# Kernel optimization log

Measured on AMD Instinct MI355X. Metric: run time of the kernel, lower is better.

Reference implementation:

```python
import jax, jax.numpy as jnp
import numpy as np

N_NODES = 50000
N_EDGES = 1600000
NODE_DIM = 64
EDGE_DIM = 32
UNITS = 64


def _glorot(key, shape):
    fan_in, fan_out = shape[0], shape[1]
    lim = jnp.sqrt(6.0 / (fan_in + fan_out))
    return jax.random.uniform(key, shape, jnp.float32, -lim, lim)


def setup_inputs() -> dict:
    key = jax.random.key(0)
    ks = jax.random.split(key, 16)
    msg_in = 2 * NODE_DIM + EDGE_DIM  # concat(sender, receiver, edge)
    upd_in = NODE_DIM + UNITS         # concat(node, aggregated)
    return {
        "node_features": jax.random.normal(ks[0], (N_NODES, NODE_DIM), jnp.float32),
        "edge_features": jax.random.normal(ks[1], (N_EDGES, EDGE_DIM), jnp.float32),
        "senders": jax.random.randint(ks[2], (N_EDGES,), 0, N_NODES, jnp.int32),
        "receivers": jnp.sort(jax.random.randint(ks[3], (N_EDGES,), 0, N_NODES, jnp.int32)),
        # message_net
        "W1": _glorot(ks[4], (msg_in, UNITS)), "b1": jnp.zeros((UNITS,), jnp.float32),
        "W2": _glorot(ks[5], (UNITS, UNITS)), "b2": jnp.zeros((UNITS,), jnp.float32),
        # attention_net
        "Wa1": _glorot(ks[6], (msg_in, UNITS)), "ba1": jnp.zeros((UNITS,), jnp.float32),
        "Wa2": _glorot(ks[7], (UNITS, 1)), "ba2": jnp.zeros((1,), jnp.float32),
        # update_net
        "Wu1": _glorot(ks[8], (upd_in, UNITS)), "bu1": jnp.zeros((UNITS,), jnp.float32),
        "Wu2": _glorot(ks[9], (UNITS, UNITS)), "bu2": jnp.zeros((UNITS,), jnp.float32),
    }


def reference(node_features, edge_features, senders, receivers,
              W1, b1, W2, b2, Wa1, ba1, Wa2, ba2, Wu1, bu1, Wu2, bu2):
    act = jax.nn.swish
    # gather + concat: [E, 2*node_dim + edge_dim]
    msg_in = jnp.concatenate(
        [node_features[senders], node_features[receivers], edge_features], axis=-1)
    # message MLP
    messages = act(msg_in @ W1 + b1) @ W2 + b2  # [E, units]
    # attention: softmax over ALL edges (axis=0), as in the original
    att_logits = act(msg_in @ Wa1 + ba1) @ Wa2 + ba2  # [E, 1]
    att = jax.nn.softmax(att_logits, axis=0)
    messages = messages * att
    # scatter-sum to receivers
    aggregated = jax.ops.segment_sum(messages, receivers, num_segments=node_features.shape[0])
    upd_in = jnp.concatenate([node_features, aggregated], axis=-1)
    return act(upd_in @ Wu1 + bu1) @ Wu2 + bu2  # [N, units]
```

## Files before the change

kernel.cpp:

```cpp
#include <hip/hip_runtime.h>
#include <cstdint>
#include <cstddef>

#define N_NODES_C 50000
#define N_EDGES_C 1600000

typedef __attribute__((ext_vector_type(8)))  short bf16x8;
typedef __attribute__((ext_vector_type(16))) float f32x16;
typedef unsigned short ushort_t;

static const size_t AGG_OFF   = 512;
static const size_t NB_OFF    = 512 + (size_t)N_NODES_C * 64 * 4;
static const size_t WIMG_OFF  = NB_OFF + (size_t)N_NODES_C * 64 * 2;
static const size_t WUIMG_OFF = WIMG_OFF + 49152;

__device__ __forceinline__ float swish_(float v) { return v / (1.0f + __expf(-v)); }

__device__ __forceinline__ unsigned short f2bf(float f) {
    unsigned int u = __float_as_uint(f);
    return (unsigned short)((u + 0x7FFFu + ((u >> 16) & 1u)) >> 16);
}
__device__ __forceinline__ unsigned int pack2(float a, float b) {
    return (unsigned int)f2bf(a) | ((unsigned int)f2bf(b) << 16);
}
__device__ __forceinline__ bf16x8 pack8(float4 a, float4 b) {
    union { uint4 u; bf16x8 v; } un;
    un.u.x = pack2(a.x, a.y); un.u.y = pack2(a.z, a.w);
    un.u.z = pack2(b.x, b.y); un.u.w = pack2(b.z, b.w);
    return un.v;
}

typedef __attribute__((address_space(3))) unsigned int lds_u32_t;
typedef const __attribute__((address_space(1))) unsigned int glb_u32_t;
__device__ __forceinline__ void glds16(const void* g, void* l) {
    __builtin_amdgcn_global_load_lds((glb_u32_t*)g, (lds_u32_t*)l, 16, 0, 0);
}

__global__ __launch_bounds__(256) void k_prep_node(const float* __restrict__ node,
                                                   ushort_t* __restrict__ node_bf)
{
    int i = blockIdx.x * 256 + threadIdx.x;
    if (i >= N_NODES_C * 64 / 8) return;
    const float4* s = (const float4*)node + (size_t)i * 2;
    float4 a = s[0], b = s[1];
    uint4 p = { pack2(a.x,a.y), pack2(a.z,a.w), pack2(b.x,b.y), pack2(b.z,b.w) };
    ((uint4*)node_bf)[i] = p;
}

__global__ __launch_bounds__(256) void k_prep_w(
    const float* __restrict__ W1, const float* __restrict__ Wa1,
    const float* __restrict__ W2, const float* __restrict__ Wu1,
    const float* __restrict__ Wu2,
    ushort_t* __restrict__ wm, ushort_t* __restrict__ wa, ushort_t* __restrict__ w2s,
    ushort_t* __restrict__ wu1t, ushort_t* __restrict__ wu2t)
{
    int b = blockIdx.x, t = threadIdx.x;
    if (b < 20) {
        int p = b * 256 + t; int n = p / 80, j = p - n * 80;
        ((unsigned int*)wm)[n * 80 + j] = pack2(W1[(size_t)(2*j) * 64 + n], W1[(size_t)(2*j+1) * 64 + n]);
    } else if (b < 40) {
        int p = (b - 20) * 256 + t; int n = p / 80, j = p - n * 80;
        ((unsigned int*)wa)[n * 80 + j] = pack2(Wa1[(size_t)(2*j) * 64 + n], Wa1[(size_t)(2*j+1) * 64 + n]);
    } else if (b < 48) {
        int p = (b - 40) * 256 + t; int n = p >> 5, q = p & 31, c = q >> 2, j = q & 3;
        ((unsigned int*)w2s)[n * 32 + ((c ^ (n & 7)) << 2) + j] =
            pack2(W2[(size_t)(c*4 + j) * 64 + n], W2[(size_t)(c*4 + j + 32) * 64 + n]);
    } else if (b < 65) {
        int p = (b - 48) * 256 + t; int n = p / 68, j = p - n * 68; int k2 = 2 * j;
        unsigned int v = (k2 < 128) ? pack2(Wu1[(size_t)k2 * 64 + n], Wu1[(size_t)(k2+1) * 64 + n]) : 0u;
        ((unsigned int*)wu1t)[n * 68 + j] = v;
    } else {
        int p = (b - 65) * 256 + t; int n = p / 36, j = p - n * 36; int k2 = 2 * j;
        unsigned int v = (k2 < 64) ? pack2(Wu2[(size_t)k2 * 64 + n], Wu2[(size_t)(k2+1) * 64 + n]) : 0u;
        ((unsigned int*)wu2t)[n * 36 + j] = v;
    }
}

__global__ __launch_bounds__(256, 2) void k_edge(
    const ushort_t* __restrict__ node_bf, const float* __restrict__ edgef,
    const int* __restrict__ senders, const int* __restrict__ receivers,
    const ushort_t* __restrict__ wimg,
    const float* __restrict__ b1, const float* __restrict__ ba1,
    const float* __restrict__ Wa2, const float* __restrict__ ba2,
    const float* __restrict__ b2,
    float* __restrict__ expsum, float* __restrict__ agg)
{
    __shared__ ushort_t SMEM[40960];
    ushort_t* As  = SMEM;
    ushort_t* Ar  = SMEM + 8192;
    ushort_t* Wm  = SMEM + 16384;
    ushort_t* Wa  = SMEM + 26624;
    ushort_t* W2s = SMEM + 36864;

    const int tid = threadIdx.x;
    const int e0 = blockIdx.x * 128;
    const int lane = tid & 63, w = tid >> 6;
    const int lr = lane & 31, hi = lane >> 5, kh = hi * 8;

    for (int c = tid; c < 2560; c += 256)
        glds16((const char*)wimg + c * 16, (char*)Wm + c * 16);
    for (int c = tid; c < 512; c += 256)
        glds16((const char*)wimg + 40960 + c * 16, (char*)W2s + c * 16);
    #pragma unroll
    for (int i = 0; i < 4; ++i) {
        int cg = tid + i * 256;
        int row = cg >> 3, c = cg & 7;
        glds16(node_bf + (size_t)senders[e0 + row] * 64 + ((c ^ (row & 7)) << 3),
               (char*)As + cg * 16);
    }
    #pragma unroll
    for (int i = 0; i < 4; ++i) {
        int cg = tid + i * 256;
        int row = cg >> 3, c = cg & 7;
        glds16(node_bf + (size_t)receivers[e0 + row] * 64 + ((c ^ (row & 7)) << 3),
               (char*)Ar + cg * 16);
    }
    bf16x8 ae0, ae1;
    {
        const float4* ep = (const float4*)(edgef + (size_t)(e0 + w * 32 + lr) * 32);
        ae0 = pack8(ep[2 * hi], ep[2 * hi + 1]);
        ae1 = pack8(ep[4 + 2 * hi], ep[4 + 2 * hi + 1]);
    }
    __syncthreads();

    f32x16 ca0, ca1, cm0, cm1;
    #pragma unroll
    for (int j = 0; j < 16; ++j) { ca0[j]=0.f; ca1[j]=0.f; cm0[j]=0.f; cm1[j]=0.f; }
    const ushort_t* asr = As + (w * 32 + lr) * 64;
    const ushort_t* arr = Ar + (w * 32 + lr) * 64;
    const ushort_t* wm0 = Wm + lr * 160 + kh;
    const ushort_t* wm1 = Wm + (32 + lr) * 160 + kh;
    const ushort_t* wa0 = Wa + lr * 160 + kh;
    const ushort_t* wa1 = Wa + (32 + lr) * 160 + kh;
    #pragma unroll
    for (int kk = 0; kk < 4; ++kk) {
        bf16x8 a = *(const bf16x8*)(asr + (((2*kk + hi) ^ (lr & 7)) << 3));
        cm0 = __builtin_amdgcn_mfma_f32_32x32x16_bf16(a, *(const bf16x8*)(wm0 + kk*16), cm0, 0,0,0);
        cm1 = __builtin_amdgcn_mfma_f32_32x32x16_bf16(a, *(const bf16x8*)(wm1 + kk*16), cm1, 0,0,0);
        ca0 = __builtin_amdgcn_mfma_f32_32x32x16_bf16(a, *(const bf16x8*)(wa0 + kk*16), ca0, 0,0,0);
        ca1 = __builtin_amdgcn_mfma_f32_32x32x16_bf16(a, *(const bf16x8*)(wa1 + kk*16), ca1, 0,0,0);
    }
    #pragma unroll
    for (int kk = 4; kk < 8; ++kk) {
        bf16x8 a = *(const bf16x8*)(arr + (((2*(kk-4) + hi) ^ (lr & 7)) << 3));
        cm0 = __builtin_amdgcn_mfma_f32_32x32x16_bf16(a, *(const bf16x8*)(wm0 + kk*16), cm0, 0,0,0);
        cm1 = __builtin_amdgcn_mfma_f32_32x32x16_bf16(a, *(const bf16x8*)(wm1 + kk*16), cm1, 0,0,0);
        ca0 = __builtin_amdgcn_mfma_f32_32x32x16_bf16(a, *(const bf16x8*)(wa0 + kk*16), ca0, 0,0,0);
        ca1 = __builtin_amdgcn_mfma_f32_32x32x16_bf16(a, *(const bf16x8*)(wa1 + kk*16), ca1, 0,0,0);
    }
    {
        bf16x8 a = ae0;
        cm0 = __builtin_amdgcn_mfma_f32_32x32x16_bf16(a, *(const bf16x8*)(wm0 + 128), cm0, 0,0,0);
        cm1 = __builtin_amdgcn_mfma_f32_32x32x16_bf16(a, *(const bf16x8*)(wm1 + 128), cm1, 0,0,0);
        ca0 = __builtin_amdgcn_mfma_f32_32x32x16_bf16(a, *(const bf16x8*)(wa0 + 128), ca0, 0,0,0);
        ca1 = __builtin_amdgcn_mfma_f32_32x32x16_bf16(a, *(const bf16x8*)(wa1 + 128), ca1, 0,0,0);
        a = ae1;
        cm0 = __builtin_amdgcn_mfma_f32_32x32x16_bf16(a, *(const bf16x8*)(wm0 + 144), cm0, 0,0,0);
        cm1 = __builtin_amdgcn_mfma_f32_32x32x16_bf16(a, *(const bf16x8*)(wm1 + 144), cm1, 0,0,0);
        ca0 = __builtin_amdgcn_mfma_f32_32x32x16_bf16(a, *(const bf16x8*)(wa0 + 144), ca0, 0,0,0);
        ca1 = __builtin_amdgcn_mfma_f32_32x32x16_bf16(a, *(const bf16x8*)(wa1 + 144), ca1, 0,0,0);
    }
    __syncthreads();

    ushort_t* H = Wa;
    const float bb0 = ba1[lr], bb1 = ba1[32 + lr];
    const float wv0 = Wa2[lr], wv1 = Wa2[32 + lr];
    #pragma unroll
    for (int t = 0; t < 16; ++t) {
        int r = (t & 3) + 8 * (t >> 2) + 4 * hi;
        *(unsigned int*)(H + (w * 32 + r) * 72 + 2 * lr) =
            pack2(swish_(ca0[t] + bb0) * wv0, swish_(ca1[t] + bb1) * wv1);
    }
    f32x16 da;
    #pragma unroll
    for (int j = 0; j < 16; ++j) da[j] = 0.f;
    bf16x8 ones;
    #pragma unroll
    for (int i = 0; i < 8; ++i) ones[i] = (short)0x3F80;
    const ushort_t* hp = H + (w * 32 + lr) * 72 + kh;
    #pragma unroll
    for (int kk = 0; kk < 4; ++kk)
        da = __builtin_amdgcn_mfma_f32_32x32x16_bf16(*(const bf16x8*)(hp + kk*16), ones, da, 0,0,0);

    const float ba2v = ba2[0];
    float p[16];
    float ps = 0.f;
    #pragma unroll
    for (int t = 0; t < 16; ++t) { p[t] = __expf(da[t] + ba2v); ps += p[t]; }
    ps += __shfl_xor(ps, 1);  ps += __shfl_xor(ps, 2);  ps += __shfl_xor(ps, 4);
    ps += __shfl_xor(ps, 8);  ps += __shfl_xor(ps, 16); ps += __shfl_xor(ps, 32);
    if (lane == 0) atomicAdd(&expsum[w * 16], ps * 0.03125f);

    const float b10 = b1[lr], b11 = b1[32 + lr];
    #pragma unroll
    for (int t = 0; t < 16; ++t) {
        int r = (t & 3) + 8 * (t >> 2) + 4 * hi;
        *(unsigned int*)(H + (w * 32 + r) * 72 + 2 * lr) =
            pack2(swish_(cm0[t] + b10), swish_(cm1[t] + b11));
    }
    f32x16 d0, d1;
    #pragma unroll
    for (int j = 0; j < 16; ++j) { d0[j] = 0.f; d1[j] = 0.f; }
    const ushort_t* q0 = W2s + lr * 64;
    const ushort_t* q1 = W2s + (32 + lr) * 64;
    #pragma unroll
    for (int kk = 0; kk < 4; ++kk) {
        bf16x8 a = *(const bf16x8*)(hp + kk * 16);
        int sw = ((2*kk + hi) ^ (lr & 7)) << 3;
        d0 = __builtin_amdgcn_mfma_f32_32x32x16_bf16(a, *(const bf16x8*)(q0 + sw), d0, 0,0,0);
        d1 = __builtin_amdgcn_mfma_f32_32x32x16_bf16(a, *(const bf16x8*)(q1 + sw), d1, 0,0,0);
    }

    float* Msc = (float*)SMEM;
    const float b20 = b2[lr], b21 = b2[32 + lr];
    #pragma unroll
    for (int t = 0; t < 16; ++t) {
        int r = (t & 3) + 8 * (t >> 2) + 4 * hi;
        float2 mv = { (d0[t] + b20) * p[t], (d1[t] + b21) * p[t] };
        *(float2*)(Msc + (w * 32 + r) * 64 + 2 * lr) = mv;
    }
    const int cj = (lane < 32) ? 2 * lane : 2 * (lane - 32) + 1;
    const int ews = e0 + w * 32;
    float acc = 0.f;
    int cur = receivers[ews];
    #pragma unroll 4
    for (int i = 0; i < 32; ++i) {
        int rr = receivers[ews + i];
        if (rr != cur) {
            atomicAdd(&agg[(size_t)cur * 64 + lane], acc);
            acc = 0.f; cur = rr;
        }
        acc += Msc[(w * 32 + i) * 64 + cj];
    }
    atomicAdd(&agg[(size_t)cur * 64 + lane], acc);
}

__global__ __launch_bounds__(256) void k_upd(
    const ushort_t* __restrict__ node_bf, const float* __restrict__ agg,
    const ushort_t* __restrict__ wuimg,
    const float* __restrict__ bu1, const float* __restrict__ bu2,
    const float* __restrict__ expsum, float* __restrict__ out)
{
    __shared__ ushort_t Un[128 * 64];
    __shared__ ushort_t Ua[128 * 64];
    __shared__ ushort_t Wu[13312];
    __shared__ ushort_t H2[128 * 72];

    const int tid = threadIdx.x;
    const int n0 = blockIdx.x * 128;

    for (int c = tid; c < 1664; c += 256)
        glds16((const char*)wuimg + c * 16, (char*)Wu + c * 16);
    #pragma unroll
    for (int i = 0; i < 4; ++i) {
        int cg = tid + i * 256;
        int row = cg >> 3, c = cg & 7;
        int n = n0 + row; if (n >= N_NODES_C) n = N_NODES_C - 1;
        glds16(node_bf + (size_t)n * 64 + ((c ^ (row & 7)) << 3), (char*)Un + cg * 16);
    }
    float z = 0.f;
    #pragma unroll
    for (int q = 0; q < 8; ++q) z += expsum[q * 16];
    const float invZ = 1.0f / z;
    {
        int row = tid >> 1, hf = tid & 1;
        int n = n0 + row; if (n >= N_NODES_C) n = N_NODES_C - 1;
        const float4* ap = (const float4*)(agg + (size_t)n * 64 + hf * 32);
        int r7 = row & 7;
        #pragma unroll
        for (int q = 0; q < 4; ++q) {
            float4 x = ap[2 * q], y = ap[2 * q + 1];
            uint4 pk = { pack2(x.x * invZ, x.y * invZ), pack2(x.z * invZ, x.w * invZ),
                         pack2(y.x * invZ, y.y * invZ), pack2(y.z * invZ, y.w * invZ) };
            int chunk = hf * 4 + q;
            *(uint4*)(Ua + row * 64 + ((chunk ^ r7) << 3)) = pk;
        }
    }
    __syncthreads();

    const int lane = tid & 63, w = tid >> 6;
    const int lr = lane & 31, hi = lane >> 5, kh = hi * 8;
    const int row_a = w * 32 + lr, r7 = lr & 7;

    f32x16 c0, c1;
    #pragma unroll
    for (int j = 0; j < 16; ++j) { c0[j] = 0.f; c1[j] = 0.f; }
    const ushort_t* un = Un + row_a * 64;
    const ushort_t* ua = Ua + row_a * 64;
    const ushort_t* w10 = Wu + lr * 136 + kh;
    const ushort_t* w11 = Wu + (32 + lr) * 136 + kh;
    #pragma unroll
    for (int kk = 0; kk < 4; ++kk) {
        bf16x8 a = *(const bf16x8*)(un + (((2*kk + hi) ^ r7) << 3));
        c0 = __builtin_amdgcn_mfma_f32_32x32x16_bf16(a, *(const bf16x8*)(w10 + kk*16), c0, 0,0,0);
        c1 = __builtin_amdgcn_mfma_f32_32x32x16_bf16(a, *(const bf16x8*)(w11 + kk*16), c1, 0,0,0);
    }
    #pragma unroll
    for (int kk = 4; kk < 8; ++kk) {
        bf16x8 a = *(const bf16x8*)(ua + (((2*(kk-4) + hi) ^ r7) << 3));
        c0 = __builtin_amdgcn_mfma_f32_32x32x16_bf16(a, *(const bf16x8*)(w10 + kk*16), c0, 0,0,0);
        c1 = __builtin_amdgcn_mfma_f32_32x32x16_bf16(a, *(const bf16x8*)(w11 + kk*16), c1, 0,0,0);
    }
    const float bb0 = bu1[lr], bb1 = bu1[32 + lr];
    #pragma unroll
    for (int t = 0; t < 16; ++t) {
        int r = (t & 3) + 8 * (t >> 2) + 4 * hi;
        int g = (w * 32 + r) * 72;
        H2[g + lr]      = f2bf(swish_(c0[t] + bb0));
        H2[g + 32 + lr] = f2bf(swish_(c1[t] + bb1));
    }
    f32x16 d0, d1;
    #pragma unroll
    for (int j = 0; j < 16; ++j) { d0[j] = 0.f; d1[j] = 0.f; }
    const ushort_t* hp = H2 + row_a * 72 + kh;
    const ushort_t* w20 = Wu + 8704 + lr * 72 + kh;
    const ushort_t* w21 = Wu + 8704 + (32 + lr) * 72 + kh;
    #pragma unroll
    for (int kk = 0; kk < 4; ++kk) {
        bf16x8 a = *(const bf16x8*)(hp + kk * 16);
        d0 = __builtin_amdgcn_mfma_f32_32x32x16_bf16(a, *(const bf16x8*)(w20 + kk*16), d0, 0,0,0);
        d1 = __builtin_amdgcn_mfma_f32_32x32x16_bf16(a, *(const bf16x8*)(w21 + kk*16), d1, 0,0,0);
    }
    const float ob0 = bu2[lr], ob1 = bu2[32 + lr];
    #pragma unroll
    for (int t = 0; t < 16; ++t) {
        int r = (t & 3) + 8 * (t >> 2) + 4 * hi;
        int g = n0 + w * 32 + r;
        if (g < N_NODES_C) {
            out[(size_t)g * 64 + lr]      = d0[t] + ob0;
            out[(size_t)g * 64 + 32 + lr] = d1[t] + ob1;
        }
    }
}

extern "C" void kernel_launch(void* const* d_in, const int* in_sizes, int n_in,
                              void* d_out, int out_size, void* d_ws, size_t ws_size,
                              hipStream_t stream)
{
    const float* node      = (const float*)d_in[0];
    const float* edgef     = (const float*)d_in[1];
    const int*   senders   = (const int*)d_in[2];
    const int*   receivers = (const int*)d_in[3];
    const float* W1  = (const float*)d_in[4];
    const float* b1  = (const float*)d_in[5];
    const float* W2  = (const float*)d_in[6];
    const float* b2  = (const float*)d_in[7];
    const float* Wa1 = (const float*)d_in[8];
    const float* ba1 = (const float*)d_in[9];
    const float* Wa2 = (const float*)d_in[10];
    const float* ba2 = (const float*)d_in[11];
    const float* Wu1 = (const float*)d_in[12];
    const float* bu1 = (const float*)d_in[13];
    const float* Wu2 = (const float*)d_in[14];
    const float* bu2 = (const float*)d_in[15];
    float* out = (float*)d_out;

    char* ws = (char*)d_ws;
    float*    expsum  = (float*)ws;
    float*    agg     = (float*)(ws + AGG_OFF);
    ushort_t* node_bf = (ushort_t*)(ws + NB_OFF);
    ushort_t* wimg    = (ushort_t*)(ws + WIMG_OFF);
    ushort_t* wuimg   = (ushort_t*)(ws + WUIMG_OFF);

    ushort_t* wm   = wimg;
    ushort_t* wa   = wimg + 10240;
    ushort_t* w2s  = wimg + 20480;
    ushort_t* wu1t = wuimg;
    ushort_t* wu2t = wuimg + 8704;

    hipMemsetAsync(ws, 0, AGG_OFF + (size_t)N_NODES_C * 64 * 4, stream);

    k_prep_node<<<(N_NODES_C * 64 / 8 + 255) / 256, 256, 0, stream>>>(node, node_bf);
    k_prep_w<<<74, 256, 0, stream>>>(W1, Wa1, W2, Wu1, Wu2, wm, wa, w2s, wu1t, wu2t);
    k_edge<<<N_EDGES_C / 128, 256, 0, stream>>>(node_bf, edgef, senders, receivers,
                                                wimg, b1, ba1, Wa2, ba2, b2, expsum, agg);
    k_upd<<<(N_NODES_C + 127) / 128, 256, 0, stream>>>(node_bf, agg, wuimg,
                                                       bu1, bu2, expsum, out);
}
```

Before: 631.0 us.

## Make edge kernel persistent with register-prefetched gathers and fused zeroing

The edge kernel becomes persistent: 512 blocks, where each wave walks a contiguous range of 32-edge tiles. Weights are loaded into LDS once per block instead of once per 128-edge block. The next tile's sender, receiver and edge features are gathered directly into registers and issued while the current tile's MFMAs run, and the exp-sum is kept per wave with one atomic at the end. The memset is folded into the node-prep kernel, and the message scratch is now bf16 in LDS rather than fp32. The risks are higher register pressure, reduced precision in the aggregated messages, and possibly lower occupancy for hiding gather latency.

```diff
diff --git a/kernel.cpp b/kernel.cpp
--- a/kernel.cpp
+++ b/kernel.cpp
@@ -4,6 +4,9 @@
 
 #define N_NODES_C 50000
 #define N_EDGES_C 1600000
+#define N_WTILES  50000
+#define N_BLOCKS  512
+#define N_GWAVES  (N_BLOCKS * 4)
 
 typedef __attribute__((ext_vector_type(8)))  short bf16x8;
 typedef __attribute__((ext_vector_type(16))) float f32x16;
@@ -12,7 +15,7 @@
 static const size_t AGG_OFF   = 512;
 static const size_t NB_OFF    = 512 + (size_t)N_NODES_C * 64 * 4;
 static const size_t WIMG_OFF  = NB_OFF + (size_t)N_NODES_C * 64 * 2;
-static const size_t WUIMG_OFF = WIMG_OFF + 49152;
+static const size_t WUIMG_OFF = WIMG_OFF + 51200;
 
 __device__ __forceinline__ float swish_(float v) { return v / (1.0f + __expf(-v)); }
 
@@ -29,6 +32,9 @@
     un.u.z = pack2(b.x, b.y); un.u.w = pack2(b.z, b.w);
     return un.v;
 }
+__device__ __forceinline__ bf16x8 as_bf8(uint4 u) {
+    union { uint4 u; bf16x8 v; } un; un.u = u; return un.v;
+}
 
 typedef __attribute__((address_space(3))) unsigned int lds_u32_t;
 typedef const __attribute__((address_space(1))) unsigned int glb_u32_t;
@@ -37,14 +43,20 @@
 }
 
 __global__ __launch_bounds__(256) void k_prep_node(const float* __restrict__ node,
-                                                   ushort_t* __restrict__ node_bf)
+                                                   ushort_t* __restrict__ node_bf,
+                                                   float* __restrict__ ws_base)
 {
     int i = blockIdx.x * 256 + threadIdx.x;
+    if (blockIdx.x == 0 && threadIdx.x < 128) ws_base[threadIdx.x] = 0.0f;
     if (i >= N_NODES_C * 64 / 8) return;
     const float4* s = (const float4*)node + (size_t)i * 2;
     float4 a = s[0], b = s[1];
     uint4 p = { pack2(a.x,a.y), pack2(a.z,a.w), pack2(b.x,b.y), pack2(b.z,b.w) };
     ((uint4*)node_bf)[i] = p;
+    float4 z = {0.f, 0.f, 0.f, 0.f};
+    float* agg = ws_base + 128;
+    ((float4*)agg)[i * 2]     = z;
+    ((float4*)agg)[i * 2 + 1] = z;
 }
 
 __global__ __launch_bounds__(256) void k_prep_w(
@@ -55,25 +67,49 @@
     ushort_t* __restrict__ wu1t, ushort_t* __restrict__ wu2t)
 {
     int b = blockIdx.x, t = threadIdx.x;
-    if (b < 20) {
-        int p = b * 256 + t; int n = p / 80, j = p - n * 80;
-        ((unsigned int*)wm)[n * 80 + j] = pack2(W1[(size_t)(2*j) * 64 + n], W1[(size_t)(2*j+1) * 64 + n]);
-    } else if (b < 40) {
-        int p = (b - 20) * 256 + t; int n = p / 80, j = p - n * 80;
-        ((unsigned int*)wa)[n * 80 + j] = pack2(Wa1[(size_t)(2*j) * 64 + n], Wa1[(size_t)(2*j+1) * 64 + n]);
-    } else if (b < 48) {
-        int p = (b - 40) * 256 + t; int n = p >> 5, q = p & 31, c = q >> 2, j = q & 3;
-        ((unsigned int*)w2s)[n * 32 + ((c ^ (n & 7)) << 2) + j] =
-            pack2(W2[(size_t)(c*4 + j) * 64 + n], W2[(size_t)(c*4 + j + 32) * 64 + n]);
-    } else if (b < 65) {
-        int p = (b - 48) * 256 + t; int n = p / 68, j = p - n * 68; int k2 = 2 * j;
-        unsigned int v = (k2 < 128) ? pack2(Wu1[(size_t)k2 * 64 + n], Wu1[(size_t)(k2+1) * 64 + n]) : 0u;
-        ((unsigned int*)wu1t)[n * 68 + j] = v;
+    if (b < 21) {
+        int p = b * 256 + t; if (p >= 5376) return;
+        int n = p / 84, j = p - n * 84;
+        unsigned int v = (j < 80) ? pack2(W1[(size_t)(2*j)*64 + n], W1[(size_t)(2*j+1)*64 + n]) : 0u;
+        ((unsigned int*)wm)[p] = v;
+    } else if (b < 42) {
+        int p = (b - 21) * 256 + t; if (p >= 5376) return;
+        int n = p / 84, j = p - n * 84;
+        unsigned int v = (j < 80) ? pack2(Wa1[(size_t)(2*j)*64 + n], Wa1[(size_t)(2*j+1)*64 + n]) : 0u;
+        ((unsigned int*)wa)[p] = v;
+    } else if (b < 50) {
+        int p = (b - 42) * 256 + t;
+        int n = p >> 5, q = p & 31, c = q >> 2, jj = q & 3;
+        ((unsigned int*)w2s)[n * 32 + ((c ^ (n & 7)) << 2) + jj] =
+            pack2(W2[(size_t)(c*4 + jj) * 64 + n], W2[(size_t)(c*4 + jj + 32) * 64 + n]);
+    } else if (b < 67) {
+        int p = (b - 50) * 256 + t; if (p >= 4352) return;
+        int n = p / 68, j = p - n * 68;
+        unsigned int v = (2*j < 128) ? pack2(Wu1[(size_t)(2*j)*64 + n], Wu1[(size_t)(2*j+1)*64 + n]) : 0u;
+        ((unsigned int*)wu1t)[p] = v;
     } else {
-        int p = (b - 65) * 256 + t; int n = p / 36, j = p - n * 36; int k2 = 2 * j;
-        unsigned int v = (k2 < 64) ? pack2(Wu2[(size_t)k2 * 64 + n], Wu2[(size_t)(k2+1) * 64 + n]) : 0u;
-        ((unsigned int*)wu2t)[n * 36 + j] = v;
-    }
+        int p = (b - 67) * 256 + t; if (p >= 2304) return;
+        int n = p / 36, j = p - n * 36;
+        unsigned int v = (2*j < 64) ? pack2(Wu2[(size_t)(2*j)*64 + n], Wu2[(size_t)(2*j+1)*64 + n]) : 0u;
+        ((unsigned int*)wu2t)[p] = v;
+    }
+}
+
+struct EBuf { uint4 sn[4]; uint4 rn[4]; float4 ef[4]; };
+
+__device__ __forceinline__ void issue_data(EBuf& b, const ushort_t* node_bf,
+                                           const float* edgef, int s, int r,
+                                           long e, int hi)
+{
+    const uint4* sp = (const uint4*)(node_bf + (size_t)s * 64);
+    const uint4* rp = (const uint4*)(node_bf + (size_t)r * 64);
+    #pragma unroll
+    for (int kk = 0; kk < 4; ++kk) b.sn[kk] = sp[2 * kk + hi];
+    #pragma unroll
+    for (int kk = 0; kk < 4; ++kk) b.rn[kk] = rp[2 * kk + hi];
+    const float4* ep = (const float4*)(edgef + (size_t)e * 32);
+    b.ef[0] = ep[2 * hi];     b.ef[1] = ep[2 * hi + 1];
+    b.ef[2] = ep[4 + 2 * hi]; b.ef[3] = ep[5 + 2 * hi];
 }
 
 __global__ __launch_bounds__(256, 2) void k_edge(
@@ -85,154 +121,157 @@
     const float* __restrict__ b2,
     float* __restrict__ expsum, float* __restrict__ agg)
 {
-    __shared__ ushort_t SMEM[40960];
-    ushort_t* As  = SMEM;
-    ushort_t* Ar  = SMEM + 8192;
-    ushort_t* Wm  = SMEM + 16384;
-    ushort_t* Wa  = SMEM + 26624;
-    ushort_t* W2s = SMEM + 36864;
+    __shared__ ushort_t SMEM[34816];
+    ushort_t* Wm  = SMEM;
+    ushort_t* Wa  = SMEM + 10752;
+    ushort_t* W2s = SMEM + 21504;
+    ushort_t* H   = SMEM + 25600;
 
     const int tid = threadIdx.x;
-    const int e0 = blockIdx.x * 128;
     const int lane = tid & 63, w = tid >> 6;
     const int lr = lane & 31, hi = lane >> 5, kh = hi * 8;
 
-    for (int c = tid; c < 2560; c += 256)
-        glds16((const char*)wimg + c * 16, (char*)Wm + c * 16);
-    for (int c = tid; c < 512; c += 256)
-        glds16((const char*)wimg + 40960 + c * 16, (char*)W2s + c * 16);
-    #pragma unroll
-    for (int i = 0; i < 4; ++i) {
-        int cg = tid + i * 256;
-        int row = cg >> 3, c = cg & 7;
-        glds16(node_bf + (size_t)senders[e0 + row] * 64 + ((c ^ (row & 7)) << 3),
-               (char*)As + cg * 16);
-    }
-    #pragma unroll
-    for (int i = 0; i < 4; ++i) {
-        int cg = tid + i * 256;
-        int row = cg >> 3, c = cg & 7;
-        glds16(node_bf + (size_t)receivers[e0 + row] * 64 + ((c ^ (row & 7)) << 3),
-               (char*)Ar + cg * 16);
-    }
-    bf16x8 ae0, ae1;
-    {
-        const float4* ep = (const float4*)(edgef + (size_t)(e0 + w * 32 + lr) * 32);
-        ae0 = pack8(ep[2 * hi], ep[2 * hi + 1]);
-        ae1 = pack8(ep[4 + 2 * hi], ep[4 + 2 * hi + 1]);
-    }
+    for (int c = tid; c < 3200; c += 256)
+        glds16((const char*)wimg + c * 16, (char*)SMEM + c * 16);
     __syncthreads();
 
-    f32x16 ca0, ca1, cm0, cm1;
-    #pragma unroll
-    for (int j = 0; j < 16; ++j) { ca0[j]=0.f; ca1[j]=0.f; cm0[j]=0.f; cm1[j]=0.f; }
-    const ushort_t* asr = As + (w * 32 + lr) * 64;
-    const ushort_t* arr = Ar + (w * 32 + lr) * 64;
-    const ushort_t* wm0 = Wm + lr * 160 + kh;
-    const ushort_t* wm1 = Wm + (32 + lr) * 160 + kh;
-    const ushort_t* wa0 = Wa + lr * 160 + kh;
-    const ushort_t* wa1 = Wa + (32 + lr) * 160 + kh;
-    #pragma unroll
-    for (int kk = 0; kk < 4; ++kk) {
-        bf16x8 a = *(const bf16x8*)(asr + (((2*kk + hi) ^ (lr & 7)) << 3));
-        cm0 = __builtin_amdgcn_mfma_f32_32x32x16_bf16(a, *(const bf16x8*)(wm0 + kk*16), cm0, 0,0,0);
-        cm1 = __builtin_amdgcn_mfma_f32_32x32x16_bf16(a, *(const bf16x8*)(wm1 + kk*16), cm1, 0,0,0);
-        ca0 = __builtin_amdgcn_mfma_f32_32x32x16_bf16(a, *(const bf16x8*)(wa0 + kk*16), ca0, 0,0,0);
-        ca1 = __builtin_amdgcn_mfma_f32_32x32x16_bf16(a, *(const bf16x8*)(wa1 + kk*16), ca1, 0,0,0);
-    }
-    #pragma unroll
-    for (int kk = 4; kk < 8; ++kk) {
-        bf16x8 a = *(const bf16x8*)(arr + (((2*(kk-4) + hi) ^ (lr & 7)) << 3));
-        cm0 = __builtin_amdgcn_mfma_f32_32x32x16_bf16(a, *(const bf16x8*)(wm0 + kk*16), cm0, 0,0,0);
-        cm1 = __builtin_amdgcn_mfma_f32_32x32x16_bf16(a, *(const bf16x8*)(wm1 + kk*16), cm1, 0,0,0);
-        ca0 = __builtin_amdgcn_mfma_f32_32x32x16_bf16(a, *(const bf16x8*)(wa0 + kk*16), ca0, 0,0,0);
-        ca1 = __builtin_amdgcn_mfma_f32_32x32x16_bf16(a, *(const bf16x8*)(wa1 + kk*16), ca1, 0,0,0);
-    }
-    {
-        bf16x8 a = ae0;
-        cm0 = __builtin_amdgcn_mfma_f32_32x32x16_bf16(a, *(const bf16x8*)(wm0 + 128), cm0, 0,0,0);
-        cm1 = __builtin_amdgcn_mfma_f32_32x32x16_bf16(a, *(const bf16x8*)(wm1 + 128), cm1, 0,0,0);
-        ca0 = __builtin_amdgcn_mfma_f32_32x32x16_bf16(a, *(const bf16x8*)(wa0 + 128), ca0, 0,0,0);
-        ca1 = __builtin_amdgcn_mfma_f32_32x32x16_bf16(a, *(const bf16x8*)(wa1 + 128), ca1, 0,0,0);
-        a = ae1;
-        cm0 = __builtin_amdgcn_mfma_f32_32x32x16_bf16(a, *(const bf16x8*)(wm0 + 144), cm0, 0,0,0);
-        cm1 = __builtin_amdgcn_mfma_f32_32x32x16_bf16(a, *(const bf16x8*)(wm1 + 144), cm1, 0,0,0);
-        ca0 = __builtin_amdgcn_mfma_f32_32x32x16_bf16(a, *(const bf16x8*)(wa0 + 144), ca0, 0,0,0);
-        ca1 = __builtin_amdgcn_mfma_f32_32x32x16_bf16(a, *(const bf16x8*)(wa1 + 144), ca1, 0,0,0);
-    }
-    __syncthreads();
-
-    ushort_t* H = Wa;
+    const int g = blockIdx.x * 4 + w;
+    const int t0 = (int)(((long)g * N_WTILES) / N_GWAVES);
+    const int t1 = (int)(((long)(g + 1) * N_WTILES) / N_GWAVES);
+
+    const ushort_t* wm0 = Wm + lr * 168 + kh;
+    const ushort_t* wm1 = Wm + (32 + lr) * 168 + kh;
+    const ushort_t* wa0 = Wa + lr * 168 + kh;
+    const ushort_t* wa1 = Wa + (32 + lr) * 168 + kh;
+    const ushort_t* q0  = W2s + lr * 64;
+    const ushort_t* q1  = W2s + (32 + lr) * 64;
+    ushort_t* Hw = H + (w * 32) * 72;
+    const ushort_t* hp = H + (w * 32 + lr) * 72 + kh;
+
     const float bb0 = ba1[lr], bb1 = ba1[32 + lr];
     const float wv0 = Wa2[lr], wv1 = Wa2[32 + lr];
-    #pragma unroll
-    for (int t = 0; t < 16; ++t) {
-        int r = (t & 3) + 8 * (t >> 2) + 4 * hi;
-        *(unsigned int*)(H + (w * 32 + r) * 72 + 2 * lr) =
-            pack2(swish_(ca0[t] + bb0) * wv0, swish_(ca1[t] + bb1) * wv1);
-    }
-    f32x16 da;
-    #pragma unroll
-    for (int j = 0; j < 16; ++j) da[j] = 0.f;
+    const float ba2v = ba2[0];
+    const float b10 = b1[lr], b11 = b1[32 + lr];
+    const float b20 = b2[lr], b21 = b2[32 + lr];
+
     bf16x8 ones;
     #pragma unroll
     for (int i = 0; i < 8; ++i) ones[i] = (short)0x3F80;
-    const ushort_t* hp = H + (w * 32 + lr) * 72 + kh;
-    #pragma unroll
-    for (int kk = 0; kk < 4; ++kk)
-        da = __builtin_amdgcn_mfma_f32_32x32x16_bf16(*(const bf16x8*)(hp + kk*16), ones, da, 0,0,0);
-
-    const float ba2v = ba2[0];
-    float p[16];
-    float ps = 0.f;
-    #pragma unroll
-    for (int t = 0; t < 16; ++t) { p[t] = __expf(da[t] + ba2v); ps += p[t]; }
-    ps += __shfl_xor(ps, 1);  ps += __shfl_xor(ps, 2);  ps += __shfl_xor(ps, 4);
-    ps += __shfl_xor(ps, 8);  ps += __shfl_xor(ps, 16); ps += __shfl_xor(ps, 32);
-    if (lane == 0) atomicAdd(&expsum[w * 16], ps * 0.03125f);
-
-    const float b10 = b1[lr], b11 = b1[32 + lr];
-    #pragma unroll
-    for (int t = 0; t < 16; ++t) {
-        int r = (t & 3) + 8 * (t >> 2) + 4 * hi;
-        *(unsigned int*)(H + (w * 32 + r) * 72 + 2 * lr) =
-            pack2(swish_(cm0[t] + b10), swish_(cm1[t] + b11));
-    }
-    f32x16 d0, d1;
-    #pragma unroll
-    for (int j = 0; j < 16; ++j) { d0[j] = 0.f; d1[j] = 0.f; }
-    const ushort_t* q0 = W2s + lr * 64;
-    const ushort_t* q1 = W2s + (32 + lr) * 64;
-    #pragma unroll
-    for (int kk = 0; kk < 4; ++kk) {
-        bf16x8 a = *(const bf16x8*)(hp + kk * 16);
-        int sw = ((2*kk + hi) ^ (lr & 7)) << 3;
-        d0 = __builtin_amdgcn_mfma_f32_32x32x16_bf16(a, *(const bf16x8*)(q0 + sw), d0, 0,0,0);
-        d1 = __builtin_amdgcn_mfma_f32_32x32x16_bf16(a, *(const bf16x8*)(q1 + sw), d1, 0,0,0);
-    }
-
-    float* Msc = (float*)SMEM;
-    const float b20 = b2[lr], b21 = b2[32 + lr];
-    #pragma unroll
-    for (int t = 0; t < 16; ++t) {
-        int r = (t & 3) + 8 * (t >> 2) + 4 * hi;
-        float2 mv = { (d0[t] + b20) * p[t], (d1[t] + b21) * p[t] };
-        *(float2*)(Msc + (w * 32 + r) * 64 + 2 * lr) = mv;
-    }
-    const int cj = (lane < 32) ? 2 * lane : 2 * (lane - 32) + 1;
-    const int ews = e0 + w * 32;
-    float acc = 0.f;
-    int cur = receivers[ews];
-    #pragma unroll 4
-    for (int i = 0; i < 32; ++i) {
-        int rr = receivers[ews + i];
-        if (rr != cur) {
-            atomicAdd(&agg[(size_t)cur * 64 + lane], acc);
-            acc = 0.f; cur = rr;
-        }
-        acc += Msc[(w * 32 + i) * 64 + cj];
-    }
-    atomicAdd(&agg[(size_t)cur * 64 + lane], acc);
+
+    EBuf buf;
+    int s_c = senders[(size_t)t0 * 32 + lr];
+    int r_c = receivers[(size_t)t0 * 32 + lr];
+    issue_data(buf, node_bf, edgef, s_c, r_c, (long)t0 * 32 + lr, hi);
+
+    float zacc = 0.0f;
+
+    for (int t = t0; t < t1; ++t) {
+        const bool more = (t + 1 < t1);
+        int s2 = 0, r2 = 0;
+        if (more) {
+            s2 = senders[(size_t)(t + 1) * 32 + lr];
+            r2 = receivers[(size_t)(t + 1) * 32 + lr];
+        }
+
+        f32x16 ca0, ca1, cm0, cm1;
+        #pragma unroll
+        for (int j = 0; j < 16; ++j) { ca0[j]=0.f; ca1[j]=0.f; cm0[j]=0.f; cm1[j]=0.f; }
+        #pragma unroll
+        for (int kk = 0; kk < 4; ++kk) {
+            bf16x8 a = as_bf8(buf.sn[kk]);
+            cm0 = __builtin_amdgcn_mfma_f32_32x32x16_bf16(a, *(const bf16x8*)(wm0 + kk*16), cm0, 0,0,0);
+            cm1 = __builtin_amdgcn_mfma_f32_32x32x16_bf16(a, *(const bf16x8*)(wm1 + kk*16), cm1, 0,0,0);
+            ca0 = __builtin_amdgcn_mfma_f32_32x32x16_bf16(a, *(const bf16x8*)(wa0 + kk*16), ca0, 0,0,0);
+            ca1 = __builtin_amdgcn_mfma_f32_32x32x16_bf16(a, *(const bf16x8*)(wa1 + kk*16), ca1, 0,0,0);
+        }
+        #pragma unroll
+        for (int kk = 4; kk < 8; ++kk) {
+            bf16x8 a = as_bf8(buf.rn[kk - 4]);
+            cm0 = __builtin_amdgcn_mfma_f32_32x32x16_bf16(a, *(const bf16x8*)(wm0 + kk*16), cm0, 0,0,0);
+            cm1 = __builtin_amdgcn_mfma_f32_32x32x16_bf16(a, *(const bf16x8*)(wm1 + kk*16), cm1, 0,0,0);
+            ca0 = __builtin_amdgcn_mfma_f32_32x32x16_bf16(a, *(const bf16x8*)(wa0 + kk*16), ca0, 0,0,0);
+            ca1 = __builtin_amdgcn_mfma_f32_32x32x16_bf16(a, *(const bf16x8*)(wa1 + kk*16), ca1, 0,0,0);
+        }
+        {
+            bf16x8 a = pack8(buf.ef[0], buf.ef[1]);
+            cm0 = __builtin_amdgcn_mfma_f32_32x32x16_bf16(a, *(const bf16x8*)(wm0 + 128), cm0, 0,0,0);
+            cm1 = __builtin_amdgcn_mfma_f32_32x32x16_bf16(a, *(const bf16x8*)(wm1 + 128), cm1, 0,0,0);
+            ca0 = __builtin_amdgcn_mfma_f32_32x32x16_bf16(a, *(const bf16x8*)(wa0 + 128), ca0, 0,0,0);
+            ca1 = __builtin_amdgcn_mfma_f32_32x32x16_bf16(a, *(const bf16x8*)(wa1 + 128), ca1, 0,0,0);
+            a = pack8(buf.ef[2], buf.ef[3]);
+            cm0 = __builtin_amdgcn_mfma_f32_32x32x16_bf16(a, *(const bf16x8*)(wm0 + 144), cm0, 0,0,0);
+            cm1 = __builtin_amdgcn_mfma_f32_32x32x16_bf16(a, *(const bf16x8*)(wm1 + 144), cm1, 0,0,0);
+            ca0 = __builtin_amdgcn_mfma_f32_32x32x16_bf16(a, *(const bf16x8*)(wa0 + 144), ca0, 0,0,0);
+            ca1 = __builtin_amdgcn_mfma_f32_32x32x16_bf16(a, *(const bf16x8*)(wa1 + 144), ca1, 0,0,0);
+        }
+
+        const int rv = r_c;
+        if (more) issue_data(buf, node_bf, edgef, s2, r2, (long)(t + 1) * 32 + lr, hi);
+        s_c = s2; r_c = r2;
+
+        #pragma unroll
+        for (int tt = 0; tt < 16; ++tt) {
+            int r = (tt & 3) + 8 * (tt >> 2) + 4 * hi;
+            *(unsigned int*)(Hw + r * 72 + 2 * lr) =
+                pack2(swish_(ca0[tt] + bb0) * wv0, swish_(ca1[tt] + bb1) * wv1);
+        }
+        f32x16 da;
+        #pragma unroll
+        for (int j = 0; j < 16; ++j) da[j] = 0.f;
+        #pragma unroll
+        for (int kk = 0; kk < 4; ++kk)
+            da = __builtin_amdgcn_mfma_f32_32x32x16_bf16(*(const bf16x8*)(hp + kk*16), ones, da, 0,0,0);
+
+        float p[16];
+        float ps = 0.f;
+        #pragma unroll
+        for (int tt = 0; tt < 16; ++tt) { p[tt] = __expf(da[tt] + ba2v); ps += p[tt]; }
+        ps += __shfl_xor(ps, 1);  ps += __shfl_xor(ps, 2);  ps += __shfl_xor(ps, 4);
+        ps += __shfl_xor(ps, 8);  ps += __shfl_xor(ps, 16); ps += __shfl_xor(ps, 32);
+        if (lane == 0) zacc += ps * 0.03125f;
+
+        #pragma unroll
+        for (int tt = 0; tt < 16; ++tt) {
+            int r = (tt & 3) + 8 * (tt >> 2) + 4 * hi;
+            *(unsigned int*)(Hw + r * 72 + 2 * lr) =
+                pack2(swish_(cm0[tt] + b10), swish_(cm1[tt] + b11));
+        }
+        f32x16 d0, d1;
+        #pragma unroll
+        for (int j = 0; j < 16; ++j) { d0[j] = 0.f; d1[j] = 0.f; }
+        #pragma unroll
+        for (int kk = 0; kk < 4; ++kk) {
+            bf16x8 a = *(const bf16x8*)(hp + kk * 16);
+            int sw = ((2*kk + hi) ^ (lr & 7)) << 3;
+            d0 = __builtin_amdgcn_mfma_f32_32x32x16_bf16(a, *(const bf16x8*)(q0 + sw), d0, 0,0,0);
+            d1 = __builtin_amdgcn_mfma_f32_32x32x16_bf16(a, *(const bf16x8*)(q1 + sw), d1, 0,0,0);
+        }
+
+        #pragma unroll
+        for (int tt = 0; tt < 16; ++tt) {
+            int r = (tt & 3) + 8 * (tt >> 2) + 4 * hi;
+            *(unsigned int*)(Hw + r * 72 + 2 * lr) =
+                pack2((d0[tt] + b20) * p[tt], (d1[tt] + b21) * p[tt]);
+        }
+
+        const int j = lane;
+        const int moff = 2 * (j & 31) + (j >> 5);
+        float acc = 0.f;
+        int cur = __shfl(rv, 0);
+        #pragma unroll 4
+        for (int i = 0; i < 32; ++i) {
+            int rr = __shfl(rv, i);
+            if (rr != cur) {
+                atomicAdd(&agg[(size_t)cur * 64 + j], acc);
+                acc = 0.f; cur = rr;
+            }
+            unsigned short mv = Hw[i * 72 + moff];
+            acc += __uint_as_float((unsigned int)mv << 16);
+        }
+        atomicAdd(&agg[(size_t)cur * 64 + j], acc);
+    }
+
+    if (lane == 0) atomicAdd(&expsum[(g & 7) * 16], zacc);
 }
 
 __global__ __launch_bounds__(256) void k_upd(
@@ -305,9 +344,9 @@
     #pragma unroll
     for (int t = 0; t < 16; ++t) {
         int r = (t & 3) + 8 * (t >> 2) + 4 * hi;
-        int g = (w * 32 + r) * 72;
-        H2[g + lr]      = f2bf(swish_(c0[t] + bb0));
-        H2[g + 32 + lr] = f2bf(swish_(c1[t] + bb1));
+        int gg = (w * 32 + r) * 72;
+        H2[gg + lr]      = f2bf(swish_(c0[t] + bb0));
+        H2[gg + 32 + lr] = f2bf(swish_(c1[t] + bb1));
     }
     f32x16 d0, d1;
     #pragma unroll
@@ -325,10 +364,10 @@
     #pragma unroll
     for (int t = 0; t < 16; ++t) {
         int r = (t & 3) + 8 * (t >> 2) + 4 * hi;
-        int g = n0 + w * 32 + r;
-        if (g < N_NODES_C) {
-            out[(size_t)g * 64 + lr]      = d0[t] + ob0;
-            out[(size_t)g * 64 + 32 + lr] = d1[t] + ob1;
+        int gg = n0 + w * 32 + r;
+        if (gg < N_NODES_C) {
+            out[(size_t)gg * 64 + lr]      = d0[t] + ob0;
+            out[(size_t)gg * 64 + 32 + lr] = d1[t] + ob1;
         }
     }
 }
@@ -363,17 +402,15 @@
     ushort_t* wuimg   = (ushort_t*)(ws + WUIMG_OFF);
 
     ushort_t* wm   = wimg;
-    ushort_t* wa   = wimg + 10240;
-    ushort_t* w2s  = wimg + 20480;
+    ushort_t* wa   = wimg + 10752;
+    ushort_t* w2s  = wimg + 21504;
     ushort_t* wu1t = wuimg;
     ushort_t* wu2t = wuimg + 8704;
 
-    hipMemsetAsync(ws, 0, AGG_OFF + (size_t)N_NODES_C * 64 * 4, stream);
-
-    k_prep_node<<<(N_NODES_C * 64 / 8 + 255) / 256, 256, 0, stream>>>(node, node_bf);
-    k_prep_w<<<74, 256, 0, stream>>>(W1, Wa1, W2, Wu1, Wu2, wm, wa, w2s, wu1t, wu2t);
-    k_edge<<<N_EDGES_C / 128, 256, 0, stream>>>(node_bf, edgef, senders, receivers,
-                                                wimg, b1, ba1, Wa2, ba2, b2, expsum, agg);
+    k_prep_node<<<(N_NODES_C * 64 / 8 + 255) / 256, 256, 0, stream>>>(node, node_bf, expsum);
+    k_prep_w<<<76, 256, 0, stream>>>(W1, Wa1, W2, Wu1, Wu2, wm, wa, w2s, wu1t, wu2t);
+    k_edge<<<N_BLOCKS, 256, 0, stream>>>(node_bf, edgef, senders, receivers,
+                                         wimg, b1, ba1, Wa2, ba2, b2, expsum, agg);
     k_upd<<<(N_NODES_C + 127) / 128, 256, 0, stream>>>(node_bf, agg, wuimg,
                                                        bu1, bu2, expsum, out);
 }
```

Result: faster. 506.4 us (-19.7%).
